# Performance work log

Hardware: AMD Instinct MI355X
Metric: run time of the kernel (lower is better)

## Reference

```python
import jax, jax.numpy as jnp
import numpy as np

BATCH = 2048
IN_DIM = 512          # group input dim
HID = 1024            # meta_output_dim = dim*2
E = 16                # meta_experts_num = num_experts*2
RANK = 2              # lora_rank
EPS = 1e-5


def setup_inputs() -> dict:
    key = jax.random.key(0)
    ks = jax.random.split(key, 8)
    x = jax.random.normal(ks[0], (BATCH, IN_DIM), jnp.float32)
    gate_states = jax.random.normal(ks[1], (BATCH, IN_DIM), jnp.float32)
    expert_indices = jnp.arange(E, dtype=jnp.int64)
    expert_weights = jax.random.normal(ks[2], (E, IN_DIM, HID), jnp.float32) * 0.02
    expert_biases = jnp.zeros((E, HID), jnp.float32)
    bn_weights = jnp.ones((E, HID), jnp.float32)
    bn_biases = jnp.zeros((E, HID), jnp.float32)
    running_mean = jax.random.normal(ks[3], (E, HID), jnp.float32) * 0.1
    running_var = jnp.abs(jax.random.normal(ks[4], (E, HID), jnp.float32)) * 0.5 + 0.5
    gate_weights = jax.random.normal(ks[5], (IN_DIM, E), jnp.float32) * 0.02
    lora_A = jax.random.normal(ks[6], (IN_DIM, RANK), jnp.float32) * 0.02
    lora_B = jax.random.normal(ks[7], (RANK, IN_DIM), jnp.float32) * 0.02
    return dict(x=x, gate_states=gate_states, expert_indices=expert_indices,
                expert_weights=expert_weights, expert_biases=expert_biases,
                bn_weights=bn_weights, bn_biases=bn_biases,
                running_mean=running_mean, running_var=running_var,
                gate_weights=gate_weights, lora_A=lora_A, lora_B=lora_B)


def reference(x, gate_states, expert_indices, expert_weights, expert_biases,
              bn_weights, bn_biases, running_mean, running_var,
              gate_weights, lora_A, lora_B):
    # LoRA feature gate (lora_gate_forward with sigmoid): x * sigmoid(x A B)
    xg = x * jax.nn.sigmoid((x @ lora_A) @ lora_B)          # [B, D]

    # Expert dispatch: gather selected expert params (home_expert_forward)
    W = expert_weights[expert_indices]                        # [E, D, H]
    b = expert_biases[expert_indices]                         # [E, H]
    h = jnp.einsum('bd,edh->ebh', xg, W) + b[:, None, :]      # [E, B, H]

    # Fused inference BatchNorm + SiLU (fused_batch_norm_silu_forward)
    inv = jax.lax.rsqrt(running_var[expert_indices] + EPS)    # [E, H]
    scale = bn_weights[expert_indices] * inv                  # [E, H]
    shift = bn_biases[expert_indices] - running_mean[expert_indices] * scale
    h = h * scale[:, None, :] + shift[:, None, :]
    h = h * jax.nn.sigmoid(h)                                 # SiLU

    # Softmax gate (gate_weights_forward) and weighted combine
    g = jax.nn.softmax(gate_states @ gate_weights, axis=-1)   # [B, E]
    out = jnp.einsum('ebh,be->bh', h, g)                      # [B, H]
    return out
```

## Files before the change

kernel.cpp:

```cpp
#include <hip/hip_runtime.h>
#include <hip/hip_bf16.h>

#define BATCH 2048
#define IN_DIM 512
#define HID 1024
#define NE 16
#define EPSV 1e-5f

typedef __bf16 bf16x8 __attribute__((ext_vector_type(8)));
typedef float floatx4 __attribute__((ext_vector_type(4)));
typedef unsigned short ushort8 __attribute__((ext_vector_type(8)));

__device__ __forceinline__ unsigned short f2bf(float f) {
  unsigned int u = __builtin_bit_cast(unsigned int, f);
  u += 0x7FFFu + ((u >> 16) & 1u);
  return (unsigned short)(u >> 16);
}

__device__ __forceinline__ int get_expert(const int* __restrict__ idx, int e) {
  bool is64 = (idx[1] == 0) && (idx[3] == 0);
  return is64 ? (int)((const long long*)idx)[e] : idx[e];
}

__device__ __forceinline__ void gld16(void* lds, const void* g) {
  __builtin_amdgcn_global_load_lds(
      (const __attribute__((address_space(1))) void*)g,
      (__attribute__((address_space(3))) void*)lds, 16, 0, 0);
}

__global__ __launch_bounds__(256) void prep_all(
    const int* __restrict__ idx, const float* __restrict__ W,
    unsigned short* __restrict__ WT,
    const float* __restrict__ x, const float* __restrict__ gs,
    const float* __restrict__ gw, const float* __restrict__ lA,
    const float* __restrict__ lB,
    unsigned short* __restrict__ xg, float* __restrict__ g,
    const float* __restrict__ bnw, const float* __restrict__ bnb,
    const float* __restrict__ rmean, const float* __restrict__ rvar,
    const float* __restrict__ ebias,
    float* __restrict__ Ac, float* __restrict__ Cc,
    float* __restrict__ out) {
  int bid = blockIdx.x;
  if (bid < 2048) {
    int e = bid >> 7, kt = (bid >> 4) & 7, ht = bid & 15;
    int ie = get_expert(idx, e);
    int k0 = kt * 64, h0 = ht * 64;
    __shared__ float tile[64][65];
    const float* Wp = W + (size_t)ie * IN_DIM * HID;
#pragma unroll
    for (int i = 0; i < 4; ++i) {
      int id = threadIdx.x + i * 256;
      int k = id >> 4, c = (id & 15) * 4;
      float4 v = *(const float4*)(Wp + (size_t)(k0 + k) * HID + h0 + c);
      tile[k][c] = v.x; tile[k][c + 1] = v.y; tile[k][c + 2] = v.z; tile[k][c + 3] = v.w;
    }
    __syncthreads();
#pragma unroll
    for (int i = 0; i < 2; ++i) {
      int id = threadIdx.x + i * 256;
      int h = id >> 3, kc = (id & 7) * 8;
      ushort8 o;
#pragma unroll
      for (int j = 0; j < 8; ++j) o[j] = f2bf(tile[kc + j][h]);
      *(ushort8*)(WT + ((size_t)e * HID + h0 + h) * IN_DIM + k0 + kc) = o;
    }
  } else if (bid < 2560) {
    int lane = threadIdx.x & 63;
    int b = (bid - 2048) * 4 + (threadIdx.x >> 6);
    const float* xrow = x + (size_t)b * IN_DIM;
    const float* grow = gs + (size_t)b * IN_DIM;
    int d0 = lane * 8;
    float4 xa = *(const float4*)(xrow + d0);
    float4 xb = *(const float4*)(xrow + d0 + 4);
    float xv[8] = {xa.x, xa.y, xa.z, xa.w, xb.x, xb.y, xb.z, xb.w};
    float4 ga = *(const float4*)(grow + d0);
    float4 gb = *(const float4*)(grow + d0 + 4);
    float gv[8] = {ga.x, ga.y, ga.z, ga.w, gb.x, gb.y, gb.z, gb.w};

    float u0 = 0.f, u1 = 0.f;
#pragma unroll
    for (int j = 0; j < 8; ++j) {
      float2 a2 = *(const float2*)(lA + (size_t)(d0 + j) * 2);
      u0 += xv[j] * a2.x;
      u1 += xv[j] * a2.y;
    }
#pragma unroll
    for (int off = 1; off < 64; off <<= 1) {
      u0 += __shfl_xor(u0, off);
      u1 += __shfl_xor(u1, off);
    }
    float ge[16];
#pragma unroll
    for (int e = 0; e < 16; ++e) ge[e] = 0.f;
#pragma unroll
    for (int j = 0; j < 8; ++j) {
      float q = gv[j];
      const float4* gwr = (const float4*)(gw + (size_t)(d0 + j) * NE);
      float4 w0 = gwr[0], w1 = gwr[1], w2 = gwr[2], w3 = gwr[3];
      ge[0] += q * w0.x; ge[1] += q * w0.y; ge[2] += q * w0.z; ge[3] += q * w0.w;
      ge[4] += q * w1.x; ge[5] += q * w1.y; ge[6] += q * w1.z; ge[7] += q * w1.w;
      ge[8] += q * w2.x; ge[9] += q * w2.y; ge[10] += q * w2.z; ge[11] += q * w2.w;
      ge[12] += q * w3.x; ge[13] += q * w3.y; ge[14] += q * w3.z; ge[15] += q * w3.w;
    }
#pragma unroll
    for (int off = 1; off < 64; off <<= 1) {
#pragma unroll
      for (int e = 0; e < 16; ++e) ge[e] += __shfl_xor(ge[e], off);
    }
    float m = ge[0];
#pragma unroll
    for (int e = 1; e < 16; ++e) m = fmaxf(m, ge[e]);
    float p[16], s = 0.f;
#pragma unroll
    for (int e = 0; e < 16; ++e) { p[e] = __expf(ge[e] - m); s += p[e]; }
    float inv = 1.f / s;
    if (lane == 0) {
      float* gout = g + (size_t)b * NE;
#pragma unroll
      for (int e = 0; e < 16; ++e) gout[e] = p[e] * inv;
    }
    ushort8 ov;
#pragma unroll
    for (int j = 0; j < 8; ++j) {
      float t = u0 * lB[d0 + j] + u1 * lB[IN_DIM + d0 + j];
      float sg = __builtin_amdgcn_rcpf(1.f + __expf(-t));
      ov[j] = f2bf(xv[j] * sg);
    }
    *(ushort8*)(xg + (size_t)b * IN_DIM + d0) = ov;
  } else if (bid < 2624) {
    int t = (bid - 2560) * 256 + threadIdx.x;
    int e = t >> 10, h = t & 1023;
    int ie = get_expert(idx, e);
    size_t o = (size_t)ie * HID + h;
    float scale = bnw[o] * rsqrtf(rvar[o] + EPSV);
    Ac[t] = scale;
    Cc[t] = (ebias[o] - rmean[o]) * scale + bnb[o];
  } else {
    int t = (bid - 2624) * 256 + threadIdx.x;
    ((float4*)out)[t] = float4{0.f, 0.f, 0.f, 0.f};
  }
}

#define BM 128
#define BN 128
#define KS 32
#define EPB 4
#define ESTRIDE ((size_t)HID * IN_DIM)

__global__ __launch_bounds__(256, 2) void moe_main(
    const unsigned short* __restrict__ xg, const unsigned short* __restrict__ WT,
    const float* __restrict__ g, const float* __restrict__ Ac,
    const float* __restrict__ Cc, float* __restrict__ out) {
  __shared__ __align__(16) unsigned short As[2][2][BM * KS];
  __shared__ __align__(16) unsigned short Bs[2][2][BN * KS];
  __shared__ float gS[BM][EPB];

  int tid = threadIdx.x;
  int lane = tid & 63, w = tid >> 6;
  int wr = w >> 1, wc = w & 1;
  int l15 = lane & 15, quad = lane >> 4;

  int bid = blockIdx.x;
  int p = bid >> 7;
  int rowb = (bid >> 3) & 15, colb = bid & 7;
  int row0 = rowb * BM, col0 = colb * BN;
  int e0 = p * EPB;

  for (int i = tid; i < BM * EPB; i += 256) {
    int r = i >> 2, e = i & 3;
    gS[r][e] = g[(size_t)(row0 + r) * NE + e0 + e];
  }

  int dr = lane >> 2, dk = (lane & 3) * 8;
  const unsigned short* gA = xg + (size_t)(row0 + w * 32 + dr) * IN_DIM + dk;
  const unsigned short* gB0 =
      WT + ((size_t)e0 * HID + col0 + w * 32 + dr) * IN_DIM + dk;

  auto dma = [&](const unsigned short* a, const unsigned short* b, int buf) {
#pragma unroll
    for (int kk = 0; kk < 2; ++kk) {
#pragma unroll
      for (int j = 0; j < 2; ++j) {
        gld16(&As[buf][kk][(w * 32 + j * 16) * KS], a + kk * KS + (size_t)j * 16 * IN_DIM);
        gld16(&Bs[buf][kk][(w * 32 + j * 16) * KS], b + kk * KS + (size_t)j * 16 * IN_DIM);
      }
    }
  };

  floatx4 acc[4][4], oacc[4][4];
#pragma unroll
  for (int rt = 0; rt < 4; ++rt)
#pragma unroll
    for (int ct = 0; ct < 4; ++ct)
#pragma unroll
      for (int r = 0; r < 4; ++r) { acc[rt][ct][r] = 0.f; oacc[rt][ct][r] = 0.f; }

  const unsigned short* gBe = gB0;
  dma(gA, gBe, 0);
  __syncthreads();

  for (int e = 0; e < EPB; ++e) {
    float Acoef[4], Ccoef[4];
#pragma unroll
    for (int ct = 0; ct < 4; ++ct) {
      int colg = col0 + wc * 64 + ct * 16 + l15;
      Acoef[ct] = Ac[(e0 + e) * HID + colg];
      Ccoef[ct] = Cc[(e0 + e) * HID + colg];
    }
#pragma unroll
    for (int s = 0; s < 8; ++s) {
      const int buf = s & 1;
      bf16x8 af[2][4], bfv[2][4];
#pragma unroll
      for (int kk = 0; kk < 2; ++kk) {
#pragma unroll
        for (int rt = 0; rt < 4; ++rt)
          af[kk][rt] = *(const bf16x8*)&As[buf][kk][(wr * 64 + rt * 16 + l15) * KS + quad * 8];
#pragma unroll
        for (int ct = 0; ct < 4; ++ct)
          bfv[kk][ct] = *(const bf16x8*)&Bs[buf][kk][(wc * 64 + ct * 16 + l15) * KS + quad * 8];
      }
      if (e < EPB - 1 || s < 7) {
        const unsigned short* an = gA + ((s + 1) & 7) * 64;
        const unsigned short* bn = (s < 7) ? (gBe + (s + 1) * 64) : (gBe + ESTRIDE);
        dma(an, bn, buf ^ 1);
      }
#pragma unroll
      for (int kk = 0; kk < 2; ++kk)
#pragma unroll
        for (int rt = 0; rt < 4; ++rt)
#pragma unroll
          for (int ct = 0; ct < 4; ++ct)
            acc[rt][ct] = __builtin_amdgcn_mfma_f32_16x16x32_bf16(af[kk][rt], bfv[kk][ct], acc[rt][ct], 0, 0, 0);
      if (s == 7) {
#pragma unroll
        for (int ct = 0; ct < 4; ++ct) {
#pragma unroll
          for (int rt = 0; rt < 4; ++rt) {
            int rb = wr * 64 + rt * 16 + quad * 4;
#pragma unroll
            for (int r = 0; r < 4; ++r) {
              float gvw = gS[rb + r][e];
              float z = Acoef[ct] * acc[rt][ct][r] + Ccoef[ct];
              float sg = __builtin_amdgcn_rcpf(1.f + __expf(-z));
              oacc[rt][ct][r] += gvw * z * sg;
              acc[rt][ct][r] = 0.f;
            }
          }
        }
      }
      __syncthreads();
    }
    gBe += ESTRIDE;
  }

#pragma unroll
  for (int rt = 0; rt < 4; ++rt)
#pragma unroll
    for (int ct = 0; ct < 4; ++ct)
#pragma unroll
      for (int r = 0; r < 4; ++r)
        atomicAdd(&out[(size_t)(row0 + wr * 64 + rt * 16 + quad * 4 + r) * HID +
                       col0 + wc * 64 + ct * 16 + l15], oacc[rt][ct][r]);
}

extern "C" void kernel_launch(void* const* d_in, const int* in_sizes, int n_in,
                              void* d_out, int out_size, void* d_ws, size_t ws_size,
                              hipStream_t stream) {
  const float* x     = (const float*)d_in[0];
  const float* gs    = (const float*)d_in[1];
  const int*   idx   = (const int*)d_in[2];
  const float* W     = (const float*)d_in[3];
  const float* ebias = (const float*)d_in[4];
  const float* bnw   = (const float*)d_in[5];
  const float* bnb   = (const float*)d_in[6];
  const float* rmean = (const float*)d_in[7];
  const float* rvar  = (const float*)d_in[8];
  const float* gw    = (const float*)d_in[9];
  const float* lA    = (const float*)d_in[10];
  const float* lB    = (const float*)d_in[11];
  float* out = (float*)d_out;

  char* ws = (char*)d_ws;
  unsigned short* WT = (unsigned short*)ws;
  unsigned short* xg = (unsigned short*)(ws + 16777216);
  float* g    = (float*)(ws + 18874368);
  float* Acf  = (float*)(ws + 19005440);
  float* Ccf  = (float*)(ws + 19070976);

  prep_all<<<dim3(4672), dim3(256), 0, stream>>>(
      idx, W, WT, x, gs, gw, lA, lB, xg, g, bnw, bnb, rmean, rvar, ebias,
      Acf, Ccf, out);
  moe_main<<<dim3((BATCH / BM) * (HID / BN) * (NE / EPB)), dim3(256), 0, stream>>>(
      xg, WT, g, Acf, Ccf, out);
}
```

Before: 197.6 us.

## Replace atomic output accumulation with split-K partial buffers and last-block reduction

Each expert-group block now stores its partial output tile to a per-group workspace slice instead of issuing float atomicAdds into the output. A per-tile counter picks the last-arriving block, which sums the other three partials with its own registers and writes the final output, so the output no longer needs zero-initialisation in the prep kernel. The MFMA inner loop also loads LDS fragments one k-substep at a time to lower register pressure. This trades atomic traffic for extra workspace writes and reads (about 32 MB) plus a threadfence and counter handshake.

New measurement: 287.6 us. 45.5% more time.

```diff
diff --git a/kernel.cpp b/kernel.cpp
--- a/kernel.cpp
+++ b/kernel.cpp
@@ -39,7 +39,7 @@
     const float* __restrict__ rmean, const float* __restrict__ rvar,
     const float* __restrict__ ebias,
     float* __restrict__ Ac, float* __restrict__ Cc,
-    float* __restrict__ out) {
+    unsigned int* __restrict__ cnt) {
   int bid = blockIdx.x;
   if (bid < 2048) {
     int e = bid >> 7, kt = (bid >> 4) & 7, ht = bid & 15;
@@ -127,7 +127,8 @@
       ov[j] = f2bf(xv[j] * sg);
     }
     *(ushort8*)(xg + (size_t)b * IN_DIM + d0) = ov;
-  } else if (bid < 2624) {
+  } else {
+    if (bid == 2560 && threadIdx.x < 128) cnt[threadIdx.x] = 0u;
     int t = (bid - 2560) * 256 + threadIdx.x;
     int e = t >> 10, h = t & 1023;
     int ie = get_expert(idx, e);
@@ -135,9 +136,6 @@
     float scale = bnw[o] * rsqrtf(rvar[o] + EPSV);
     Ac[t] = scale;
     Cc[t] = (ebias[o] - rmean[o]) * scale + bnb[o];
-  } else {
-    int t = (bid - 2624) * 256 + threadIdx.x;
-    ((float4*)out)[t] = float4{0.f, 0.f, 0.f, 0.f};
   }
 }
 
@@ -146,14 +144,17 @@
 #define KS 32
 #define EPB 4
 #define ESTRIDE ((size_t)HID * IN_DIM)
+#define OUTSZ ((size_t)BATCH * HID)
 
 __global__ __launch_bounds__(256, 2) void moe_main(
     const unsigned short* __restrict__ xg, const unsigned short* __restrict__ WT,
     const float* __restrict__ g, const float* __restrict__ Ac,
-    const float* __restrict__ Cc, float* __restrict__ out) {
+    const float* __restrict__ Cc, float* __restrict__ sws,
+    unsigned int* __restrict__ cnt, float* __restrict__ out) {
   __shared__ __align__(16) unsigned short As[2][2][BM * KS];
   __shared__ __align__(16) unsigned short Bs[2][2][BN * KS];
   __shared__ float gS[BM][EPB];
+  __shared__ unsigned int sLast;
 
   int tid = threadIdx.x;
   int lane = tid & 63, w = tid >> 6;
@@ -210,28 +211,26 @@
 #pragma unroll
     for (int s = 0; s < 8; ++s) {
       const int buf = s & 1;
-      bf16x8 af[2][4], bfv[2][4];
-#pragma unroll
-      for (int kk = 0; kk < 2; ++kk) {
-#pragma unroll
-        for (int rt = 0; rt < 4; ++rt)
-          af[kk][rt] = *(const bf16x8*)&As[buf][kk][(wr * 64 + rt * 16 + l15) * KS + quad * 8];
-#pragma unroll
-        for (int ct = 0; ct < 4; ++ct)
-          bfv[kk][ct] = *(const bf16x8*)&Bs[buf][kk][(wc * 64 + ct * 16 + l15) * KS + quad * 8];
-      }
       if (e < EPB - 1 || s < 7) {
         const unsigned short* an = gA + ((s + 1) & 7) * 64;
         const unsigned short* bn = (s < 7) ? (gBe + (s + 1) * 64) : (gBe + ESTRIDE);
         dma(an, bn, buf ^ 1);
       }
 #pragma unroll
-      for (int kk = 0; kk < 2; ++kk)
+      for (int kk = 0; kk < 2; ++kk) {
+        bf16x8 af[4], bfv[4];
 #pragma unroll
         for (int rt = 0; rt < 4; ++rt)
+          af[rt] = *(const bf16x8*)&As[buf][kk][(wr * 64 + rt * 16 + l15) * KS + quad * 8];
+#pragma unroll
+        for (int ct = 0; ct < 4; ++ct)
+          bfv[ct] = *(const bf16x8*)&Bs[buf][kk][(wc * 64 + ct * 16 + l15) * KS + quad * 8];
+#pragma unroll
+        for (int rt = 0; rt < 4; ++rt)
 #pragma unroll
           for (int ct = 0; ct < 4; ++ct)
-            acc[rt][ct] = __builtin_amdgcn_mfma_f32_16x16x32_bf16(af[kk][rt], bfv[kk][ct], acc[rt][ct], 0, 0, 0);
+            acc[rt][ct] = __builtin_amdgcn_mfma_f32_16x16x32_bf16(af[rt], bfv[ct], acc[rt][ct], 0, 0, 0);
+      }
       if (s == 7) {
 #pragma unroll
         for (int ct = 0; ct < 4; ++ct) {
@@ -254,14 +253,36 @@
     gBe += ESTRIDE;
   }
 
+  float* sout = sws + (size_t)p * OUTSZ;
 #pragma unroll
   for (int rt = 0; rt < 4; ++rt)
 #pragma unroll
     for (int ct = 0; ct < 4; ++ct)
 #pragma unroll
       for (int r = 0; r < 4; ++r)
-        atomicAdd(&out[(size_t)(row0 + wr * 64 + rt * 16 + quad * 4 + r) * HID +
-                       col0 + wc * 64 + ct * 16 + l15], oacc[rt][ct][r]);
+        sout[(size_t)(row0 + wr * 64 + rt * 16 + quad * 4 + r) * HID +
+             col0 + wc * 64 + ct * 16 + l15] = oacc[rt][ct][r];
+
+  __threadfence();
+  if (tid == 0) sLast = atomicAdd(&cnt[rowb * 8 + colb], 1u);
+  __syncthreads();
+  if (sLast == 3u) {
+    __threadfence();
+#pragma unroll
+    for (int rt = 0; rt < 4; ++rt)
+#pragma unroll
+      for (int ct = 0; ct < 4; ++ct)
+#pragma unroll
+        for (int r = 0; r < 4; ++r) {
+          size_t off = (size_t)(row0 + wr * 64 + rt * 16 + quad * 4 + r) * HID +
+                       col0 + wc * 64 + ct * 16 + l15;
+          float v = oacc[rt][ct][r];
+#pragma unroll
+          for (int q = 0; q < 4; ++q)
+            if (q != p) v += sws[(size_t)q * OUTSZ + off];
+          out[off] = v;
+        }
+  }
 }
 
 extern "C" void kernel_launch(void* const* d_in, const int* in_sizes, int n_in,
@@ -287,10 +308,12 @@
   float* g    = (float*)(ws + 18874368);
   float* Acf  = (float*)(ws + 19005440);
   float* Ccf  = (float*)(ws + 19070976);
-
-  prep_all<<<dim3(4672), dim3(256), 0, stream>>>(
+  float* sws  = (float*)(ws + 19136512);
+  unsigned int* cnt = (unsigned int*)(ws + 52690944);
+
+  prep_all<<<dim3(2624), dim3(256), 0, stream>>>(
       idx, W, WT, x, gs, gw, lA, lB, xg, g, bnw, bnb, rmean, rvar, ebias,
-      Acf, Ccf, out);
+      Acf, Ccf, cnt);
   moe_main<<<dim3((BATCH / BM) * (HID / BN) * (NE / EPB)), dim3(256), 0, stream>>>(
-      xg, WT, g, Acf, Ccf, out);
-}
+      xg, WT, g, Acf, Ccf, sws, cnt, out);
+}
```
